# Optimization experiments

Hardware: AMD Instinct MI355X
Metric: run time of the kernel (lower is better)

## Reference

```python
import jax, jax.numpy as jnp
import numpy as np

B, C_IN, C_H, C_OUT, H, W = 2, 512, 512, 512, 14, 14


def setup_inputs() -> dict:
    key = jax.random.key(0)
    ks = jax.random.split(key, 6)
    s_in = 1.0 / np.sqrt(C_IN + C_H)   # torch Linear init bound for in_linear
    s_out = 1.0 / np.sqrt(C_H)          # torch Linear init bound for out_linear
    return {
        "input": jax.random.normal(ks[0], (B, C_IN, H, W), jnp.float32),
        # in_linear weight (C_H, C_IN + C_H) split into x-part and h-part
        "Wx": jax.random.uniform(ks[1], (C_H, C_IN), jnp.float32, -s_in, s_in),
        "Wh": jax.random.uniform(ks[2], (C_H, C_H), jnp.float32, -s_in, s_in),
        "b_in": jax.random.uniform(ks[3], (C_H,), jnp.float32, -s_in, s_in),
        "Wo": jax.random.uniform(ks[4], (C_OUT, C_H), jnp.float32, -s_out, s_out),
        "b_out": jax.random.uniform(ks[5], (C_OUT,), jnp.float32, -s_out, s_out),
    }


def reference(input, Wx, Wh, b_in, Wo, b_out):
    Bn, _, Hn, Wn = input.shape
    hid = Wh.shape[0]
    # four scan directions = four flips of the input (outputs are summed in
    # flipped coordinates, exactly as the original torch code does -- no unflip)
    x_modes = jnp.stack([
        input,
        jnp.flip(input, 3),
        jnp.flip(input, 2),
        jnp.flip(jnp.flip(input, 2), 3),
    ])  # (4, B, C_IN, H, W)
    rows = jnp.arange(Hn)
    cols = jnp.arange(Wn)

    def run_mode(x):
        # x-contribution of in_linear, shared by every (i,j) in the window
        a = jnp.einsum('hc,bcxy->bhxy', Wx, x) + b_in[None, :, None, None]

        def step(h, p):
            px, py = p // Wn, p % Wn
            # h_vivj over the full grid; cells outside the causal window hold
            # h == 0 and are masked out of the sum below (softmax is per-pixel
            # over channels, so no cross-pixel contamination)
            z = jax.nn.relu(a[:, :, px, py][:, :, None, None]
                            + jnp.einsum('ch,bhxy->bcxy', Wh, h))
            sm = jax.nn.softmax(z, axis=1)  # Softmax(dim=1): over channels
            mask = (rows[:, None] <= px) & (cols[None, :] <= py)  # (H, W)
            h_vi = jnp.sum(z * sm * mask, axis=(2, 3))  # (B, hid)
            h = h.at[:, :, px, py].set(h_vi)
            y_vi = h_vi @ Wo.T + b_out
            return h, y_vi

        h0 = jnp.zeros((Bn, hid, Hn, Wn), input.dtype)
        _, ys = jax.lax.scan(step, h0, jnp.arange(Hn * Wn))
        # ys: (H*W, B, C_OUT) -> (B, C_OUT, H, W) in raster order
        return ys.reshape(Hn, Wn, Bn, -1).transpose(2, 3, 0, 1)

    y = jax.vmap(run_mode)(x_modes).sum(axis=0)  # sum over the 4 directions
    return jax.nn.softmax(y, axis=1)
```

## Files before the change

### kernel.cpp

```cpp
#include <hip/hip_runtime.h>
#include <hip/hip_bf16.h>

#define BB 2
#define CC 512
#define HH 14
#define WW 14
#define PP 196
#define NSEQ 8
#define NSLICE 8
#define NWORK (14 * NSLICE)
#define FW 16
#define NZERO (3 * PP * FW)
#define ALL8 0x0101010101010101ull


__global__ __launch_bounds__(256) void prep(
    const float* __restrict__ Wx, const float* __restrict__ X,
    const float* __restrict__ b_in, const float* __restrict__ Wh,
    const float* __restrict__ Wo,
    float* __restrict__ A, float* __restrict__ WhT, float* __restrict__ WoT,
    unsigned* __restrict__ cnts ) {
    __shared__ float Ws[32][33], Xs[32][33];
    int bid = blockIdx.x;
    int t = threadIdx.x;
    if (bid < 224) {
        int z = bid / 112, rem = bid % 112;
        int c0 = (rem % 16) * 32, p0 = (rem / 16) * 32;
        int tx = t % 32, ty = t / 32;
        int pl = (t % 16) * 2, cl = (t / 16) * 2;
        float acc[2][2] = {{0.f,0.f},{0.f,0.f}};
        for (int k0 = 0; k0 < CC; k0 += 32) {
            #pragma unroll
            for (int r = 0; r < 4; ++r)
                Ws[ty + 8*r][tx] = Wx[(size_t)(c0 + ty + 8*r) * CC + k0 + tx];
            #pragma unroll
            for (int r = 0; r < 4; ++r) {
                int p = p0 + tx, k = k0 + ty + 8*r;
                Xs[ty + 8*r][tx] = (p < PP) ? X[((size_t)z * CC + k) * PP + p] : 0.f;
            }
            __syncthreads();
            #pragma unroll
            for (int k = 0; k < 32; ++k) {
                float w0 = Ws[cl][k], w1 = Ws[cl+1][k];
                float x0 = Xs[k][pl], x1 = Xs[k][pl+1];
                acc[0][0] += w0*x0; acc[0][1] += w0*x1;
                acc[1][0] += w1*x0; acc[1][1] += w1*x1;
            }
            __syncthreads();
        }
        #pragma unroll
        for (int i = 0; i < 2; ++i)
            #pragma unroll
            for (int j = 0; j < 2; ++j) {
                int c = c0 + cl + i, p = p0 + pl + j;
                if (p < PP) A[((size_t)z * PP + p) * CC + c] = acc[i][j] + b_in[c];
            }
    } else if (bid < 736) {
        int tid = bid - 224;
        const float* src = (tid < 256) ? Wh : Wo;
        float* dst = (tid < 256) ? WhT : WoT;
        tid &= 255;
        int c0 = (tid % 16) * 32, k0 = (tid / 16) * 32;
        int tx = t % 32, ty = t / 32;
        #pragma unroll
        for (int r = 0; r < 4; ++r)
            Ws[ty + 8*r][tx] = src[(size_t)(c0 + ty + 8*r) * CC + k0 + tx];
        __syncthreads();
        #pragma unroll
        for (int r = 0; r < 4; ++r)
            dst[(size_t)(k0 + ty + 8*r) * CC + c0 + tx] = Ws[tx][ty + 8*r];
    } else {
        for (int i = t; i < NZERO; i += 256) cnts[i] = 0u;
    }
}

__device__ __forceinline__ unsigned long long flag8_ld(const unsigned char* f) {
    return __hip_atomic_load((const unsigned long long*)f, __ATOMIC_RELAXED,
                             __HIP_MEMORY_SCOPE_AGENT);
}
__device__ __forceinline__ void flag_st(unsigned char* f) {
    __hip_atomic_store(f, (unsigned char)1, __ATOMIC_RELAXED,
                       __HIP_MEMORY_SCOPE_AGENT);
}
__device__ __forceinline__ float ldf_agent(const float* p) {
    return __hip_atomic_load(p, __ATOMIC_RELAXED, __HIP_MEMORY_SCOPE_AGENT);
}
__device__ __forceinline__ void store_wt(float* p, float v) {
    __hip_atomic_store(p, v, __ATOMIC_RELAXED, __HIP_MEMORY_SCOPE_AGENT);
}

__device__ __forceinline__ void pix(const float4 E0, const float4 E1,
                                    const float* ar, const float* er, float* hacc) {
    float ee[8] = {E0.x,E0.y,E0.z,E0.w,E1.x,E1.y,E1.z,E1.w};
    float ds = 0.f, tl[8];
    #pragma unroll
    for (int j = 0; j < 8; ++j) {
        float sv = ar[j] + __logf(ee[j]);
        float pv = er[j] * ee[j];
        ds += fmaxf(pv, 1.0f);
        tl[j] = fmaxf(sv, 0.0f) * pv;
    }
    #pragma unroll
    for (int off = 32; off; off >>= 1) ds += __shfl_xor(ds, off, 64);
    float rd = 1.0f / ds;
    #pragma unroll
    for (int j = 0; j < 8; ++j) hacc[j] += tl[j] * rd;
}

__device__ __forceinline__ void proc_row(const float* __restrict__ rowp, int n,
                                         const float* ar, const float* er, float* hacc) {
    float4 cur[4][2];
    int y = 0, curn = (n < 4) ? n : 4;
    #pragma unroll
    for (int i = 0; i < 4; ++i) if (i < curn) {
        cur[i][0] = *(const float4*)(rowp + (size_t)i * CC);
        cur[i][1] = *(const float4*)(rowp + (size_t)i * CC + 256);
    }
    while (true) {
        int yn = y + curn;
        int rem = n - yn;
        int nextn = (rem < 4) ? rem : 4;
        float4 nxt[4][2];
        #pragma unroll
        for (int i = 0; i < 4; ++i) if (i < nextn) {
            nxt[i][0] = *(const float4*)(rowp + (size_t)(yn + i) * CC);
            nxt[i][1] = *(const float4*)(rowp + (size_t)(yn + i) * CC + 256);
        }
        #pragma unroll
        for (int i = 0; i < 4; ++i) if (i < curn)
            pix(cur[i][0], cur[i][1], ar, er, hacc);
        if (nextn <= 0) break;
        #pragma unroll
        for (int i = 0; i < 4; ++i) if (i < nextn) {
            cur[i][0] = nxt[i][0]; cur[i][1] = nxt[i][1];
        }
        curn = nextn; y = yn;
    }
}

__global__ __launch_bounds__(512, 2) void rnn_dataflow(
    const float* __restrict__ A, const float* __restrict__ WhT,
    float* __restrict__ E, float* __restrict__ h_bulk,
    float* __restrict__ h_t, float* __restrict__ TLN,
    float* __restrict__ TLW, float* __restrict__ dsAcc,
    unsigned char* __restrict__ uflag, unsigned char* __restrict__ hflag,
    const float* __restrict__ WoT, const float* __restrict__ b_out,
    float* __restrict__ out) {
    __shared__ __align__(16) float hT8[CC * 8];
    __shared__ __align__(16) float up[8 * 576];
    __shared__ unsigned mbox;
    __shared__ unsigned pf;
    int bid = blockIdx.x;
    int t = threadIdx.x;
    int lane = t & 63, wv = t >> 6;

    if (bid < NWORK) {
        int px = bid >> 3, w = bid & 7;
        int ch = w * 64 + lane;
        int m = wv >> 1, b = wv & 1;
        float wreg2[64];
        #pragma unroll
        for (int kk = 0; kk < 64; ++kk)
            wreg2[kk] = WhT[(size_t)(wv * 64 + kk) * CC + ch];
        __builtin_amdgcn_s_setprio(1);

        float hb[8];
        float tnr[8], dsNr[8];
        bool hb_ok = false;
        bool n_ok  = false;

        for (int py = 0; py < WW; ++py) {
            int cell = px * WW + py;
            int cellN = cell - WW, cellW = cell - 1;

            float aSr = 0.f, aWr = 0.f;
            if (px < HH - 1) {
                int fi = (m & 2) ? (HH - 2 - px) : (px + 1);
                int fj = (m & 1) ? (WW - 1 - py) : py;
                aSr = A[((size_t)b * PP + fi * WW + fj) * CC + ch];
            }
            if (py < WW - 1) {
                int fi = (m & 2) ? (HH - 1 - px) : px;
                int fj = (m & 1) ? (WW - 2 - py) : (py + 1);
                aWr = A[((size_t)b * PP + fi * WW + fj) * CC + ch];
            }

            if (!hb_ok) {
                if (wv == 0 && lane == 0)
                    while (flag8_ld(hflag + (size_t)cell * 64) != ALL8)
                        __builtin_amdgcn_s_sleep(1);
                __syncthreads();
                asm volatile("" ::: "memory");
                #pragma unroll
                for (int s = 0; s < 8; ++s)
                    hb[s] = h_bulk[((size_t)cell * NSEQ + s) * CC + t];
            }

            if (wv == 0) {
                while (true) {
                    unsigned ok = 1u;
                    if (lane == 0)      { if (py > 0) ok = (flag8_ld(uflag + (size_t)cellW * 64) == ALL8); }
                    else if (lane == 1) { if (px > 0 && !n_ok) ok = (flag8_ld(uflag + (size_t)cellN * 64) == ALL8); }
                    if (__ballot(ok != 0u) == ~0ull) break;
                    __builtin_amdgcn_s_sleep(1);
                }
            }
            __syncthreads();
            asm volatile("" ::: "memory");

            if (px > 0) {
                if (!n_ok) {
                    #pragma unroll
                    for (int i = 0; i < 8; ++i)
                        dsNr[i] = ldf_agent(&dsAcc[(size_t)cell * 16 + i]);
                    #pragma unroll
                    for (int s = 0; s < 8; ++s)
                        tnr[s] = ldf_agent(&TLN[((size_t)cell * NSEQ + s) * CC + t]);
                }
                #pragma unroll
                for (int s = 0; s < 8; ++s)
                    hb[s] += tnr[s] * __builtin_amdgcn_rcpf(dsNr[s]);
            }
            if (py > 0) {
                float dsw[8], tw[8];
                #pragma unroll
                for (int i = 0; i < 8; ++i)
                    dsw[i] = ldf_agent(&dsAcc[(size_t)cell * 16 + 8 + i]);
                #pragma unroll
                for (int s = 0; s < 8; ++s)
                    tw[s] = ldf_agent(&TLW[((size_t)cell * NSEQ + s) * CC + t]);
                #pragma unroll
                for (int s = 0; s < 8; ++s)
                    hb[s] += tw[s] * __builtin_amdgcn_rcpf(dsw[s]);
            }
            if (wv == w) {
                #pragma unroll
                for (int s = 0; s < 8; ++s)
                    store_wt(&h_t[((size_t)cell * NSEQ + s) * CC + t], hb[s]);
            }
            *(float4*)&hT8[t * 8]     = make_float4(hb[0], hb[1], hb[2], hb[3]);
            *(float4*)&hT8[t * 8 + 4] = make_float4(hb[4], hb[5], hb[6], hb[7]);
            if (cell == PP - 1) {
                __builtin_amdgcn_s_waitcnt(0);
                asm volatile("" ::: "memory");
                if (wv == w && lane == 0)
                    flag_st(uflag + (size_t)cell * 64 + w);
                break;
            }

            float acc[8] = {0.f,0.f,0.f,0.f,0.f,0.f,0.f,0.f};
            const float* hp = hT8 + (wv << 9);
            #pragma unroll
            for (int kk = 0; kk < 64; ++kk) {
                float4 h0 = *(const float4*)(hp + kk * 8);
                float4 h1 = *(const float4*)(hp + kk * 8 + 4);
                float wvv = wreg2[kk];
                acc[0] += wvv * h0.x; acc[1] += wvv * h0.y;
                acc[2] += wvv * h0.z; acc[3] += wvv * h0.w;
                acc[4] += wvv * h1.x; acc[5] += wvv * h1.y;
                acc[6] += wvv * h1.z; acc[7] += wvv * h1.w;
            }
            #pragma unroll
            for (int s = 0; s < 8; ++s)
                up[wv * 576 + lane * 9 + s] = acc[s];
            __syncthreads();

            {
                float U = up[lane * 9 + wv];
                #pragma unroll
                for (int w2 = 1; w2 < 8; ++w2) U += up[w2 * 576 + lane * 9 + wv];
                float Ev = __expf(U);
                store_wt(&E[((size_t)wv * PP + cell) * CC + ch], Ev);
                float pdS = 0.f, pdW = 0.f;
                if (px < HH - 1) {
                    float pv = __expf(aSr) * Ev;
                    store_wt(&TLN[((size_t)(cell + WW) * NSEQ + wv) * CC + ch],
                             fmaxf(aSr + U, 0.f) * pv);
                    pdS = fmaxf(pv, 1.f);
                }
                if (py < WW - 1) {
                    float pv = __expf(aWr) * Ev;
                    store_wt(&TLW[((size_t)(cell + 1) * NSEQ + wv) * CC + ch],
                             fmaxf(aWr + U, 0.f) * pv);
                    pdW = fmaxf(pv, 1.f);
                }
                #pragma unroll
                for (int off = 32; off; off >>= 1) {
                    pdS += __shfl_xor(pdS, off, 64);
                    pdW += __shfl_xor(pdW, off, 64);
                }
                if (lane == 0) {
                    if (px < HH - 1)
                        unsafeAtomicAdd(&dsAcc[(size_t)(cell + WW) * 16 + wv], pdS);
                    if (py < WW - 1)
                        unsafeAtomicAdd(&dsAcc[(size_t)(cell + 1) * 16 + 8 + wv], pdW);
                }
            }

            if (t == 0) {
                unsigned v = 0u;
                if (py + 1 < WW) {
                    if (flag8_ld(hflag + (size_t)(cell + 1) * 64) == ALL8) v |= 1u;
                    if (px > 0 &&
                        flag8_ld(uflag + (size_t)(cellN + 1) * 64) == ALL8) v |= 2u;
                }
                pf = v;
            }

            __syncthreads();
            if (t == 0) flag_st(uflag + (size_t)cell * 64 + w);

            hb_ok = false; n_ok = false;
            if (py + 1 < WW) {
                unsigned v = pf;
                if (v & 1u) {
                    #pragma unroll
                    for (int s = 0; s < 8; ++s)
                        hb[s] = h_bulk[((size_t)(cell + 1) * NSEQ + s) * CC + t];
                    hb_ok = true;
                }
                if (v & 2u) {
                    #pragma unroll
                    for (int i = 0; i < 8; ++i)
                        dsNr[i] = ldf_agent(&dsAcc[(size_t)(cell + 1) * 16 + i]);
                    #pragma unroll
                    for (int s = 0; s < 8; ++s)
                        tnr[s] = ldf_agent(&TLN[((size_t)(cell + 1) * NSEQ + s) * CC + t]);
                    n_ok = true;
                }
            }
        }
    } else if (bid < NWORK + PP) {
        int cell = bid - NWORK;
        int px = cell / WW, py = cell % WW;
        int s = wv, m = s >> 1, b = s & 1;
        int fi = (m & 2) ? (HH-1-px) : px;
        int fj = (m & 1) ? (WW-1-py) : py;
        int cb = lane * 4;

        if (t == 0) mbox = 0u;
        __syncthreads();

        const float* acur = A + ((size_t)b * PP + fi * WW + fj) * CC;
        float4 a0 = *(const float4*)(acur + cb);
        float4 a1 = *(const float4*)(acur + cb + 256);
        float ar[8] = {a0.x,a0.y,a0.z,a0.w,a1.x,a1.y,a1.z,a1.w};
        float er[8];
        #pragma unroll
        for (int j = 0; j < 8; ++j) er[j] = __expf(ar[j]);
        float hacc[8] = {0.f,0.f,0.f,0.f,0.f,0.f,0.f,0.f};

        {
            float ds = 0.f, tl[8];
            #pragma unroll
            for (int j = 0; j < 8; ++j) {
                float pv = er[j];
                ds += fmaxf(pv, 1.0f);
                tl[j] = fmaxf(ar[j], 0.0f) * pv;
            }
            #pragma unroll
            for (int off = 32; off; off >>= 1) ds += __shfl_xor(ds, off, 64);
            float rd = 1.0f / ds;
            #pragma unroll
            for (int j = 0; j < 8; ++j) hacc[j] += tl[j] * rd;
        }

        const float* Eb = E + (size_t)s * PP * CC;
        int sx = lane >> 1, sph = lane & 1;
        int gate = -1;
        if (sx <= px) {
            int L = (sx <= px-2) ? py : ((sx == px-1) ? py-1 : py-2);
            if (L >= 0) {
                if (L <= 2) { if (sph == 0) gate = sx * WW + L; }
                else gate = sx * WW + (sph ? L : (L - 3));
            }
        }
        unsigned pend = (unsigned)__ballot(gate >= 0);

        if (wv == 0) {
            unsigned done = 0u;
            while (pend) {
                bool rdy = true;
                if (gate >= 0 && ((pend >> lane) & 1u))
                    rdy = (flag8_ld(uflag + (size_t)gate * 64) == ALL8);
                unsigned newly = pend & (unsigned)__ballot(rdy);
                if (!newly) { __builtin_amdgcn_s_sleep(2); continue; }
                done |= newly;
                __hip_atomic_store(&mbox, done, __ATOMIC_RELAXED,
                                   __HIP_MEMORY_SCOPE_WORKGROUP);
                asm volatile("" ::: "memory");
                unsigned go = newly;
                while (go) {
                    int sl = __ffs(go) - 1; go &= go - 1;
                    int xx = sl >> 1;
                    int L = (xx <= px-2) ? py : ((xx == px-1) ? py-1 : py-2);
                    int yy0 = 0, yy1 = L;
                    if (L > 2) { if (sl & 1) yy0 = L - 2; else yy1 = L - 3; }
                    proc_row(Eb + (size_t)(xx * WW + yy0) * CC + cb,
                             yy1 - yy0 + 1, ar, er, hacc);
                }
                pend &= ~newly;
            }
        } else {
            while (pend) {
                unsigned d = __hip_atomic_load(&mbox, __ATOMIC_RELAXED,
                                               __HIP_MEMORY_SCOPE_WORKGROUP);
                unsigned newly = d & pend;
                if (!newly) { __builtin_amdgcn_s_sleep(2); continue; }
                asm volatile("" ::: "memory");
                unsigned go = newly;
                while (go) {
                    int sl = __ffs(go) - 1; go &= go - 1;
                    int xx = sl >> 1;
                    int L = (xx <= px-2) ? py : ((xx == px-1) ? py-1 : py-2);
                    int yy0 = 0, yy1 = L;
                    if (L > 2) { if (sl & 1) yy0 = L - 2; else yy1 = L - 3; }
                    proc_row(Eb + (size_t)(xx * WW + yy0) * CC + cb,
                             yy1 - yy0 + 1, ar, er, hacc);
                }
                pend &= ~newly;
            }
        }

        float* hp = h_bulk + ((size_t)cell * NSEQ + s) * CC;
        #pragma unroll
        for (int j = 0; j < 4; ++j) {
            store_wt(hp + cb + j,       hacc[j]);
            store_wt(hp + cb + 256 + j, hacc[4 + j]);
        }
        __builtin_amdgcn_s_waitcnt(0);
        asm volatile("" ::: "memory");
        if (lane == 0) flag_st(hflag + (size_t)cell * 64 + s);
    } else {
        int p = bid - NWORK - PP;
        float2* hs2 = (float2*)hT8;
        float (*redm)[2] = (float (*)[2])up;
        float (*reds)[2] = (float (*)[2])(up + 64);

        if (t == 0)
            while (flag8_ld(uflag + (size_t)p * 64) != ALL8)
                __builtin_amdgcn_s_sleep(8);
        __syncthreads();
        asm volatile("" ::: "memory");

        {
            float v[8];
            #pragma unroll
            for (int s = 0; s < 8; ++s)
                v[s] = ldf_agent(&h_t[((size_t)p * NSEQ + s) * CC + t]);
            hs2[t] = make_float2(v[0]+v[2]+v[4]+v[6], v[1]+v[3]+v[5]+v[7]);
        }
        __syncthreads();

        float y0 = 4.0f * b_out[t], y1 = y0;
        for (int k0 = 0; k0 < CC; k0 += 8) {
            float wk[8];
            #pragma unroll
            for (int j = 0; j < 8; ++j)
                wk[j] = WoT[(size_t)(k0 + j) * CC + t];
            #pragma unroll
            for (int j = 0; j < 8; ++j) {
                float2 hk = hs2[k0 + j];
                y0 += wk[j] * hk.x;
                y1 += wk[j] * hk.y;
            }
        }

        float m0 = y0, m1 = y1;
        #pragma unroll
        for (int off = 32; off; off >>= 1) {
            m0 = fmaxf(m0, __shfl_xor(m0, off, 64));
            m1 = fmaxf(m1, __shfl_xor(m1, off, 64));
        }
        if (lane == 0) { redm[wv][0] = m0; redm[wv][1] = m1; }
        __syncthreads();
        float gm0 = redm[0][0], gm1 = redm[0][1];
        #pragma unroll
        for (int i = 1; i < 8; ++i) {
            gm0 = fmaxf(gm0, redm[i][0]);
            gm1 = fmaxf(gm1, redm[i][1]);
        }
        float e0 = expf(y0 - gm0), e1 = expf(y1 - gm1);
        float s0 = e0, s1 = e1;
        #pragma unroll
        for (int off = 32; off; off >>= 1) {
            s0 += __shfl_xor(s0, off, 64);
            s1 += __shfl_xor(s1, off, 64);
        }
        if (lane == 0) { reds[wv][0] = s0; reds[wv][1] = s1; }
        __syncthreads();
        float t0 = 0.f, t1 = 0.f;
        #pragma unroll
        for (int i = 0; i < 8; ++i) { t0 += reds[i][0]; t1 += reds[i][1]; }
        out[((size_t)0 * CC + t) * PP + p] = e0 * (1.0f / t0);
        out[((size_t)1 * CC + t) * PP + p] = e1 * (1.0f / t1);
    }
}

extern "C" void kernel_launch(void* const* d_in, const int* in_sizes, int n_in,
                              void* d_out, int out_size, void* d_ws, size_t ws_size,
                              hipStream_t stream) {
    const float* X     = (const float*)d_in[0];
    const float* Wx    = (const float*)d_in[1];
    const float* Wh    = (const float*)d_in[2];
    const float* b_in  = (const float*)d_in[3];
    const float* Wo    = (const float*)d_in[4];
    const float* b_out = (const float*)d_in[5];
    float* out = (float*)d_out;

    float* ws     = (float*)d_ws;
    float* WhT    = ws;
    float* A      = WhT    + 262144;
    float* E      = A      + 200704;
    float* h_bulk = E      + 802816;
    float* h_t    = h_bulk + 802816;
    float* TLN    = h_t    + 802816;
    float* TLW    = TLN    + 802816;
    float* WoT    = TLW    + 802816;
    unsigned char* uflag = (unsigned char*)(WoT + 262144);
    unsigned char* hflag = uflag + PP * 64;
    float* dsAcc = (float*)(hflag + PP * 64);

    hipLaunchKernelGGL(prep, dim3(737), dim3(256), 0, stream,
                       Wx, X, b_in, Wh, Wo, A, WhT, WoT, (unsigned*)uflag);
    hipLaunchKernelGGL(rnn_dataflow, dim3(NWORK + PP + PP), dim3(512), 0, stream,
                       A, WhT, E, h_bulk, h_t, TLN, TLW, dsAcc, uflag, hflag,
                       WoT, b_out, out);
}
```

Before: 319.4 us.

## Fuse prep into dataflow kernel with atomic counter barrier and batched consumers

Folds the prep kernel (A projection and weight transposes) into the main persistent kernel as its first 736 blocks. Downstream blocks spin on an atomic completion counter instead of waiting for a kernel boundary. The zeroing of flags moves to a hipMemsetAsync. Output consumer blocks are halved to 98, each handling two pixels, with staggered sleep delays to cut polling contention. The aim is to remove a launch gap and free CUs for the workers, at the cost of spin-wait risk and larger blocks running prep with half their threads idle.

```diff
diff --git a/kernel.cpp b/kernel.cpp
--- a/kernel.cpp
+++ b/kernel.cpp
@@ -9,70 +9,10 @@
 #define NSEQ 8
 #define NSLICE 8
 #define NWORK (14 * NSLICE)
-#define FW 16
-#define NZERO (3 * PP * FW)
+#define PREPB 736
+#define NCONS 98
 #define ALL8 0x0101010101010101ull
 
-
-__global__ __launch_bounds__(256) void prep(
-    const float* __restrict__ Wx, const float* __restrict__ X,
-    const float* __restrict__ b_in, const float* __restrict__ Wh,
-    const float* __restrict__ Wo,
-    float* __restrict__ A, float* __restrict__ WhT, float* __restrict__ WoT,
-    unsigned* __restrict__ cnts ) {
-    __shared__ float Ws[32][33], Xs[32][33];
-    int bid = blockIdx.x;
-    int t = threadIdx.x;
-    if (bid < 224) {
-        int z = bid / 112, rem = bid % 112;
-        int c0 = (rem % 16) * 32, p0 = (rem / 16) * 32;
-        int tx = t % 32, ty = t / 32;
-        int pl = (t % 16) * 2, cl = (t / 16) * 2;
-        float acc[2][2] = {{0.f,0.f},{0.f,0.f}};
-        for (int k0 = 0; k0 < CC; k0 += 32) {
-            #pragma unroll
-            for (int r = 0; r < 4; ++r)
-                Ws[ty + 8*r][tx] = Wx[(size_t)(c0 + ty + 8*r) * CC + k0 + tx];
-            #pragma unroll
-            for (int r = 0; r < 4; ++r) {
-                int p = p0 + tx, k = k0 + ty + 8*r;
-                Xs[ty + 8*r][tx] = (p < PP) ? X[((size_t)z * CC + k) * PP + p] : 0.f;
-            }
-            __syncthreads();
-            #pragma unroll
-            for (int k = 0; k < 32; ++k) {
-                float w0 = Ws[cl][k], w1 = Ws[cl+1][k];
-                float x0 = Xs[k][pl], x1 = Xs[k][pl+1];
-                acc[0][0] += w0*x0; acc[0][1] += w0*x1;
-                acc[1][0] += w1*x0; acc[1][1] += w1*x1;
-            }
-            __syncthreads();
-        }
-        #pragma unroll
-        for (int i = 0; i < 2; ++i)
-            #pragma unroll
-            for (int j = 0; j < 2; ++j) {
-                int c = c0 + cl + i, p = p0 + pl + j;
-                if (p < PP) A[((size_t)z * PP + p) * CC + c] = acc[i][j] + b_in[c];
-            }
-    } else if (bid < 736) {
-        int tid = bid - 224;
-        const float* src = (tid < 256) ? Wh : Wo;
-        float* dst = (tid < 256) ? WhT : WoT;
-        tid &= 255;
-        int c0 = (tid % 16) * 32, k0 = (tid / 16) * 32;
-        int tx = t % 32, ty = t / 32;
-        #pragma unroll
-        for (int r = 0; r < 4; ++r)
-            Ws[ty + 8*r][tx] = src[(size_t)(c0 + ty + 8*r) * CC + k0 + tx];
-        __syncthreads();
-        #pragma unroll
-        for (int r = 0; r < 4; ++r)
-            dst[(size_t)(k0 + ty + 8*r) * CC + c0 + tx] = Ws[tx][ty + 8*r];
-    } else {
-        for (int i = t; i < NZERO; i += 256) cnts[i] = 0u;
-    }
-}
 
 __device__ __forceinline__ unsigned long long flag8_ld(const unsigned char* f) {
     return __hip_atomic_load((const unsigned long long*)f, __ATOMIC_RELAXED,
@@ -139,13 +79,15 @@
 }
 
 __global__ __launch_bounds__(512, 2) void rnn_dataflow(
-    const float* __restrict__ A, const float* __restrict__ WhT,
+    const float* __restrict__ Wx, const float* __restrict__ X,
+    const float* __restrict__ b_in, const float* __restrict__ Wh,
+    const float* __restrict__ Wo, const float* __restrict__ b_out,
+    float* __restrict__ A, float* __restrict__ WhT, float* __restrict__ WoT,
     float* __restrict__ E, float* __restrict__ h_bulk,
     float* __restrict__ h_t, float* __restrict__ TLN,
     float* __restrict__ TLW, float* __restrict__ dsAcc,
     unsigned char* __restrict__ uflag, unsigned char* __restrict__ hflag,
-    const float* __restrict__ WoT, const float* __restrict__ b_out,
-    float* __restrict__ out) {
+    unsigned* __restrict__ prepcnt, float* __restrict__ out) {
     __shared__ __align__(16) float hT8[CC * 8];
     __shared__ __align__(16) float up[8 * 576];
     __shared__ unsigned mbox;
@@ -154,8 +96,86 @@
     int t = threadIdx.x;
     int lane = t & 63, wv = t >> 6;
 
-    if (bid < NWORK) {
-        int px = bid >> 3, w = bid & 7;
+    if (bid < 224) {
+        float* WsA = hT8;
+        float* XsA = hT8 + 1056;
+        int z = bid / 112, rem = bid % 112;
+        int c0 = (rem % 16) * 32, p0 = (rem / 16) * 32;
+        int tt = t & 255;
+        int tx = tt % 32, ty = tt / 32;
+        int pl = (tt % 16) * 2, cl = (tt / 16) * 2;
+        float acc[2][2] = {{0.f,0.f},{0.f,0.f}};
+        for (int k0 = 0; k0 < CC; k0 += 32) {
+            if (t < 256) {
+                #pragma unroll
+                for (int r = 0; r < 4; ++r)
+                    WsA[(ty + 8*r) * 33 + tx] = Wx[(size_t)(c0 + ty + 8*r) * CC + k0 + tx];
+                #pragma unroll
+                for (int r = 0; r < 4; ++r) {
+                    int p = p0 + tx, k = k0 + ty + 8*r;
+                    XsA[(ty + 8*r) * 33 + tx] = (p < PP) ? X[((size_t)z * CC + k) * PP + p] : 0.f;
+                }
+            }
+            __syncthreads();
+            if (t < 256) {
+                #pragma unroll
+                for (int k = 0; k < 32; ++k) {
+                    float w0 = WsA[cl * 33 + k], w1 = WsA[(cl+1) * 33 + k];
+                    float x0 = XsA[k * 33 + pl], x1 = XsA[k * 33 + pl + 1];
+                    acc[0][0] += w0*x0; acc[0][1] += w0*x1;
+                    acc[1][0] += w1*x0; acc[1][1] += w1*x1;
+                }
+            }
+            __syncthreads();
+        }
+        if (t < 256) {
+            #pragma unroll
+            for (int i = 0; i < 2; ++i)
+                #pragma unroll
+                for (int j = 0; j < 2; ++j) {
+                    int c = c0 + cl + i, p = p0 + pl + j;
+                    if (p < PP)
+                        store_wt(&A[((size_t)z * PP + p) * CC + c], acc[i][j] + b_in[c]);
+                }
+        }
+        __builtin_amdgcn_s_waitcnt(0);
+        __syncthreads();
+        if (t == 0) atomicAdd(prepcnt, 1u);
+    } else if (bid < PREPB) {
+        float* WsA = hT8;
+        int tid = bid - 224;
+        const float* src = (tid < 256) ? Wh : Wo;
+        float* dst = (tid < 256) ? WhT : WoT;
+        tid &= 255;
+        int c0 = (tid % 16) * 32, k0 = (tid / 16) * 32;
+        int tt = t & 255;
+        int tx = tt % 32, ty = tt / 32;
+        if (t < 256) {
+            #pragma unroll
+            for (int r = 0; r < 4; ++r)
+                WsA[(ty + 8*r) * 33 + tx] = src[(size_t)(c0 + ty + 8*r) * CC + k0 + tx];
+        }
+        __syncthreads();
+        if (t < 256) {
+            #pragma unroll
+            for (int r = 0; r < 4; ++r)
+                store_wt(&dst[(size_t)(k0 + ty + 8*r) * CC + c0 + tx],
+                         WsA[tx * 33 + ty + 8*r]);
+        }
+        __builtin_amdgcn_s_waitcnt(0);
+        __syncthreads();
+        if (t == 0) atomicAdd(prepcnt, 1u);
+    } else {
+        if (t == 0)
+            while (__hip_atomic_load(prepcnt, __ATOMIC_RELAXED,
+                                     __HIP_MEMORY_SCOPE_AGENT) < (unsigned)PREPB)
+                __builtin_amdgcn_s_sleep(16);
+        __syncthreads();
+        asm volatile("" ::: "memory");
+        int rb = bid - PREPB;
+
+        if (rb < NWORK) {
+        int px = rb >> 3, w = rb & 7;
         int ch = w * 64 + lane;
         int m = wv >> 1, b = wv & 1;
         float wreg2[64];
@@ -330,8 +350,8 @@
                 }
             }
         }
-    } else if (bid < NWORK + PP) {
-        int cell = bid - NWORK;
+        } else if (rb < NWORK + PP) {
+        int cell = rb - NWORK;
         int px = cell / WW, py = cell % WW;
         int s = wv, m = s >> 1, b = s & 1;
         int fi = (m & 2) ? (HH-1-px) : px;
@@ -431,69 +451,85 @@
         __builtin_amdgcn_s_waitcnt(0);
         asm volatile("" ::: "memory");
         if (lane == 0) flag_st(hflag + (size_t)cell * 64 + s);
-    } else {
-        int p = bid - NWORK - PP;
+        } else {
+        int cj = rb - NWORK - PP;
         float2* hs2 = (float2*)hT8;
         float (*redm)[2] = (float (*)[2])up;
         float (*reds)[2] = (float (*)[2])(up + 64);
 
-        if (t == 0)
-            while (flag8_ld(uflag + (size_t)p * 64) != ALL8)
-                __builtin_amdgcn_s_sleep(8);
-        __syncthreads();
-        asm volatile("" ::: "memory");
-
-        {
-            float v[8];
-            #pragma unroll
-            for (int s = 0; s < 8; ++s)
-                v[s] = ldf_agent(&h_t[((size_t)p * NSEQ + s) * CC + t]);
-            hs2[t] = make_float2(v[0]+v[2]+v[4]+v[6], v[1]+v[3]+v[5]+v[7]);
-        }
-        __syncthreads();
-
-        float y0 = 4.0f * b_out[t], y1 = y0;
-        for (int k0 = 0; k0 < CC; k0 += 8) {
-            float wk[8];
-            #pragma unroll
-            for (int j = 0; j < 8; ++j)
-                wk[j] = WoT[(size_t)(k0 + j) * CC + t];
-            #pragma unroll
-            for (int j = 0; j < 8; ++j) {
-                float2 hk = hs2[k0 + j];
-                y0 += wk[j] * hk.x;
-                y1 += wk[j] * hk.y;
-            }
-        }
-
-        float m0 = y0, m1 = y1;
-        #pragma unroll
-        for (int off = 32; off; off >>= 1) {
-            m0 = fmaxf(m0, __shfl_xor(m0, off, 64));
-            m1 = fmaxf(m1, __shfl_xor(m1, off, 64));
-        }
-        if (lane == 0) { redm[wv][0] = m0; redm[wv][1] = m1; }
-        __syncthreads();
-        float gm0 = redm[0][0], gm1 = redm[0][1];
-        #pragma unroll
-        for (int i = 1; i < 8; ++i) {
-            gm0 = fmaxf(gm0, redm[i][0]);
-            gm1 = fmaxf(gm1, redm[i][1]);
-        }
-        float e0 = expf(y0 - gm0), e1 = expf(y1 - gm1);
-        float s0 = e0, s1 = e1;
-        #pragma unroll
-        for (int off = 32; off; off >>= 1) {
-            s0 += __shfl_xor(s0, off, 64);
-            s1 += __shfl_xor(s1, off, 64);
-        }
-        if (lane == 0) { reds[wv][0] = s0; reds[wv][1] = s1; }
-        __syncthreads();
-        float t0 = 0.f, t1 = 0.f;
-        #pragma unroll
-        for (int i = 0; i < 8; ++i) { t0 += reds[i][0]; t1 += reds[i][1]; }
-        out[((size_t)0 * CC + t) * PP + p] = e0 * (1.0f / t0);
-        out[((size_t)1 * CC + t) * PP + p] = e1 * (1.0f / t1);
+        for (int pi = 0; pi < 2; ++pi) {
+            int p = cj + pi * NCONS;
+            if (t == 0) {
+                if (pi == 0) {
+                    int d = p / WW + p % WW;
+                    for (int i = 0; i < 2 * d; ++i)
+                        __builtin_amdgcn_s_sleep(127);
+                }
+                if (p >= PP - 2 * WW) {
+                    while (flag8_ld(uflag + (size_t)p * 64) != ALL8)
+                        __builtin_amdgcn_s_sleep(2);
+                } else {
+                    while (flag8_ld(uflag + (size_t)p * 64) != ALL8)
+                        __builtin_amdgcn_s_sleep(32);
+                }
+            }
+            __syncthreads();
+            asm volatile("" ::: "memory");
+
+            {
+                float v[8];
+                #pragma unroll
+                for (int s = 0; s < 8; ++s)
+                    v[s] = ldf_agent(&h_t[((size_t)p * NSEQ + s) * CC + t]);
+                hs2[t] = make_float2(v[0]+v[2]+v[4]+v[6], v[1]+v[3]+v[5]+v[7]);
+            }
+            __syncthreads();
+
+            float y0 = 4.0f * b_out[t], y1 = y0;
+            for (int k0 = 0; k0 < CC; k0 += 8) {
+                float wk[8];
+                #pragma unroll
+                for (int j = 0; j < 8; ++j)
+                    wk[j] = WoT[(size_t)(k0 + j) * CC + t];
+                #pragma unroll
+                for (int j = 0; j < 8; ++j) {
+                    float2 hk = hs2[k0 + j];
+                    y0 += wk[j] * hk.x;
+                    y1 += wk[j] * hk.y;
+                }
+            }
+
+            float m0 = y0, m1 = y1;
+            #pragma unroll
+            for (int off = 32; off; off >>= 1) {
+                m0 = fmaxf(m0, __shfl_xor(m0, off, 64));
+                m1 = fmaxf(m1, __shfl_xor(m1, off, 64));
+            }
+            if (lane == 0) { redm[wv][0] = m0; redm[wv][1] = m1; }
+            __syncthreads();
+            float gm0 = redm[0][0], gm1 = redm[0][1];
+            #pragma unroll
+            for (int i = 1; i < 8; ++i) {
+                gm0 = fmaxf(gm0, redm[i][0]);
+                gm1 = fmaxf(gm1, redm[i][1]);
+            }
+            float e0 = expf(y0 - gm0), e1 = expf(y1 - gm1);
+            float s0 = e0, s1 = e1;
+            #pragma unroll
+            for (int off = 32; off; off >>= 1) {
+                s0 += __shfl_xor(s0, off, 64);
+                s1 += __shfl_xor(s1, off, 64);
+            }
+            if (lane == 0) { reds[wv][0] = s0; reds[wv][1] = s1; }
+            __syncthreads();
+            float t0 = 0.f, t1 = 0.f;
+            #pragma unroll
+            for (int i = 0; i < 8; ++i) { t0 += reds[i][0]; t1 += reds[i][1]; }
+            out[((size_t)0 * CC + t) * PP + p] = e0 * (1.0f / t0);
+            out[((size_t)1 * CC + t) * PP + p] = e1 * (1.0f / t1);
+            __syncthreads();
+        }
+        }
     }
 }
 
@@ -520,10 +556,13 @@
     unsigned char* uflag = (unsigned char*)(WoT + 262144);
     unsigned char* hflag = uflag + PP * 64;
     float* dsAcc = (float*)(hflag + PP * 64);
-
-    hipLaunchKernelGGL(prep, dim3(737), dim3(256), 0, stream,
-                       Wx, X, b_in, Wh, Wo, A, WhT, WoT, (unsigned*)uflag);
-    hipLaunchKernelGGL(rnn_dataflow, dim3(NWORK + PP + PP), dim3(512), 0, stream,
-                       A, WhT, E, h_bulk, h_t, TLN, TLW, dsAcc, uflag, hflag,
-                       WoT, b_out, out);
-}
+    unsigned* prepcnt = (unsigned*)(dsAcc + PP * 16);
+
+    hipMemsetAsync(uflag, 0, (size_t)PP * 64 * 2 + (size_t)PP * 16 * 4 + 64,
+                   stream);
+    hipLaunchKernelGGL(rnn_dataflow, dim3(PREPB + NWORK + PP + NCONS),
+                       dim3(512), 0, stream,
+                       Wx, X, b_in, Wh, Wo, b_out,
+                       A, WhT, WoT, E, h_bulk, h_t, TLN, TLW, dsAcc,
+                       uflag, hflag, prepcnt, out);
+}
```

Measured after the change: 354.9 us. 1.11x slower.

## Pair output pixels per consumer block and zero flags via memset

Applied to the files above, without the earlier changes.

Each output-projection consumer block now handles two pixels, so every WoT column load is reused across four accumulators and the consumer block count is halved. Flag and counter zeroing moves out of the prep kernel into a hipMemsetAsync. This cuts repeated WoT reads and the number of resident spinning consumer blocks. In exchange, each block must wait for both pixels to finish, which may delay the epilogue tail, and the memset adds one extra launch.

```diff
diff --git a/kernel.cpp b/kernel.cpp
--- a/kernel.cpp
+++ b/kernel.cpp
@@ -9,8 +9,7 @@
 #define NSEQ 8
 #define NSLICE 8
 #define NWORK (14 * NSLICE)
-#define FW 16
-#define NZERO (3 * PP * FW)
+#define NCONS 98
 #define ALL8 0x0101010101010101ull
 
 
@@ -18,8 +17,7 @@
     const float* __restrict__ Wx, const float* __restrict__ X,
     const float* __restrict__ b_in, const float* __restrict__ Wh,
     const float* __restrict__ Wo,
-    float* __restrict__ A, float* __restrict__ WhT, float* __restrict__ WoT,
-    unsigned* __restrict__ cnts ) {
+    float* __restrict__ A, float* __restrict__ WhT, float* __restrict__ WoT) {
     __shared__ float Ws[32][33], Xs[32][33];
     int bid = blockIdx.x;
     int t = threadIdx.x;
@@ -55,7 +53,7 @@
                 int c = c0 + cl + i, p = p0 + pl + j;
                 if (p < PP) A[((size_t)z * PP + p) * CC + c] = acc[i][j] + b_in[c];
             }
-    } else if (bid < 736) {
+    } else {
         int tid = bid - 224;
         const float* src = (tid < 256) ? Wh : Wo;
         float* dst = (tid < 256) ? WhT : WoT;
@@ -69,8 +67,6 @@
         #pragma unroll
         for (int r = 0; r < 4; ++r)
             dst[(size_t)(k0 + ty + 8*r) * CC + c0 + tx] = Ws[tx][ty + 8*r];
-    } else {
-        for (int i = t; i < NZERO; i += 256) cnts[i] = 0u;
     }
 }
 
@@ -432,14 +428,19 @@
         asm volatile("" ::: "memory");
         if (lane == 0) flag_st(hflag + (size_t)cell * 64 + s);
     } else {
-        int p = bid - NWORK - PP;
-        float2* hs2 = (float2*)hT8;
-        float (*redm)[2] = (float (*)[2])up;
-        float (*reds)[2] = (float (*)[2])(up + 64);
-
-        if (t == 0)
-            while (flag8_ld(uflag + (size_t)p * 64) != ALL8)
+        int j2 = bid - NWORK - PP;
+        int pA = 2 * j2, pB = 2 * j2 + 1;
+        float2* hsA = (float2*)hT8;
+        float2* hsB = (float2*)(hT8 + 1024);
+        float (*redm)[4] = (float (*)[4])up;
+        float (*reds)[4] = (float (*)[4])(up + 64);
+
+        if (t == 0) {
+            while (flag8_ld(uflag + (size_t)pA * 64) != ALL8)
                 __builtin_amdgcn_s_sleep(8);
+            while (flag8_ld(uflag + (size_t)pB * 64) != ALL8)
+                __builtin_amdgcn_s_sleep(8);
+        }
         __syncthreads();
         asm volatile("" ::: "memory");
 
@@ -447,12 +448,17 @@
             float v[8];
             #pragma unroll
             for (int s = 0; s < 8; ++s)
-                v[s] = ldf_agent(&h_t[((size_t)p * NSEQ + s) * CC + t]);
-            hs2[t] = make_float2(v[0]+v[2]+v[4]+v[6], v[1]+v[3]+v[5]+v[7]);
+                v[s] = ldf_agent(&h_t[((size_t)pA * NSEQ + s) * CC + t]);
+            hsA[t] = make_float2(v[0]+v[2]+v[4]+v[6], v[1]+v[3]+v[5]+v[7]);
+            #pragma unroll
+            for (int s = 0; s < 8; ++s)
+                v[s] = ldf_agent(&h_t[((size_t)pB * NSEQ + s) * CC + t]);
+            hsB[t] = make_float2(v[0]+v[2]+v[4]+v[6], v[1]+v[3]+v[5]+v[7]);
         }
         __syncthreads();
 
-        float y0 = 4.0f * b_out[t], y1 = y0;
+        float bb = 4.0f * b_out[t];
+        float ya0 = bb, ya1 = bb, yb0 = bb, yb1 = bb;
         for (int k0 = 0; k0 < CC; k0 += 8) {
             float wk[8];
             #pragma unroll
@@ -460,40 +466,50 @@
                 wk[j] = WoT[(size_t)(k0 + j) * CC + t];
             #pragma unroll
             for (int j = 0; j < 8; ++j) {
-                float2 hk = hs2[k0 + j];
-                y0 += wk[j] * hk.x;
-                y1 += wk[j] * hk.y;
-            }
-        }
-
-        float m0 = y0, m1 = y1;
+                float2 ha = hsA[k0 + j], hb2 = hsB[k0 + j];
+                ya0 += wk[j] * ha.x;  ya1 += wk[j] * ha.y;
+                yb0 += wk[j] * hb2.x; yb1 += wk[j] * hb2.y;
+            }
+        }
+
+        float m0 = ya0, m1 = ya1, m2 = yb0, m3 = yb1;
         #pragma unroll
         for (int off = 32; off; off >>= 1) {
             m0 = fmaxf(m0, __shfl_xor(m0, off, 64));
             m1 = fmaxf(m1, __shfl_xor(m1, off, 64));
-        }
-        if (lane == 0) { redm[wv][0] = m0; redm[wv][1] = m1; }
+            m2 = fmaxf(m2, __shfl_xor(m2, off, 64));
+            m3 = fmaxf(m3, __shfl_xor(m3, off, 64));
+        }
+        if (lane == 0) { redm[wv][0]=m0; redm[wv][1]=m1; redm[wv][2]=m2; redm[wv][3]=m3; }
         __syncthreads();
-        float gm0 = redm[0][0], gm1 = redm[0][1];
+        float g0 = redm[0][0], g1 = redm[0][1], g2 = redm[0][2], g3 = redm[0][3];
         #pragma unroll
         for (int i = 1; i < 8; ++i) {
-            gm0 = fmaxf(gm0, redm[i][0]);
-            gm1 = fmaxf(gm1, redm[i][1]);
-        }
-        float e0 = expf(y0 - gm0), e1 = expf(y1 - gm1);
-        float s0 = e0, s1 = e1;
+            g0 = fmaxf(g0, redm[i][0]); g1 = fmaxf(g1, redm[i][1]);
+            g2 = fmaxf(g2, redm[i][2]); g3 = fmaxf(g3, redm[i][3]);
+        }
+        float e0 = expf(ya0 - g0), e1 = expf(ya1 - g1);
+        float e2 = expf(yb0 - g2), e3 = expf(yb1 - g3);
+        float s0 = e0, s1 = e1, s2 = e2, s3 = e3;
         #pragma unroll
         for (int off = 32; off; off >>= 1) {
             s0 += __shfl_xor(s0, off, 64);
             s1 += __shfl_xor(s1, off, 64);
-        }
-        if (lane == 0) { reds[wv][0] = s0; reds[wv][1] = s1; }
+            s2 += __shfl_xor(s2, off, 64);
+            s3 += __shfl_xor(s3, off, 64);
+        }
+        if (lane == 0) { reds[wv][0]=s0; reds[wv][1]=s1; reds[wv][2]=s2; reds[wv][3]=s3; }
         __syncthreads();
-        float t0 = 0.f, t1 = 0.f;
-        #pragma unroll
-        for (int i = 0; i < 8; ++i) { t0 += reds[i][0]; t1 += reds[i][1]; }
-        out[((size_t)0 * CC + t) * PP + p] = e0 * (1.0f / t0);
-        out[((size_t)1 * CC + t) * PP + p] = e1 * (1.0f / t1);
+        float t0 = 0.f, t1 = 0.f, t2 = 0.f, t3 = 0.f;
+        #pragma unroll
+        for (int i = 0; i < 8; ++i) {
+            t0 += reds[i][0]; t1 += reds[i][1];
+            t2 += reds[i][2]; t3 += reds[i][3];
+        }
+        out[((size_t)0 * CC + t) * PP + pA] = e0 * (1.0f / t0);
+        out[((size_t)1 * CC + t) * PP + pA] = e1 * (1.0f / t1);
+        out[((size_t)0 * CC + t) * PP + pB] = e2 * (1.0f / t2);
+        out[((size_t)1 * CC + t) * PP + pB] = e3 * (1.0f / t3);
     }
 }
 
@@ -521,9 +537,10 @@
     unsigned char* hflag = uflag + PP * 64;
     float* dsAcc = (float*)(hflag + PP * 64);
 
-    hipLaunchKernelGGL(prep, dim3(737), dim3(256), 0, stream,
-                       Wx, X, b_in, Wh, Wo, A, WhT, WoT, (unsigned*)uflag);
-    hipLaunchKernelGGL(rnn_dataflow, dim3(NWORK + PP + PP), dim3(512), 0, stream,
+    hipMemsetAsync(uflag, 0, (size_t)PP * 64 * 2 + (size_t)PP * 16 * 4, stream);
+    hipLaunchKernelGGL(prep, dim3(736), dim3(256), 0, stream,
+                       Wx, X, b_in, Wh, Wo, A, WhT, WoT);
+    hipLaunchKernelGGL(rnn_dataflow, dim3(NWORK + PP + NCONS), dim3(512), 0, stream,
                        A, WhT, E, h_bulk, h_t, TLN, TLW, dsAcc, uflag, hflag,
                        WoT, b_out, out);
 }
```

New measurement: 327.1 us. 1.02x slower.
